# Kernel tuning notes

Measured on AMD Instinct MI355X. Metric: run time of the kernel, lower is better.

The kernel has to match this reference:

```python
import jax, jax.numpy as jnp
import numpy as np

B, S, D = 4, 2048, 1024
H, HD = 16, 64
F = 4096
EPS = 1e-5


def layer_norm(x, gamma, beta):
    mu = jnp.mean(x, axis=-1, keepdims=True)
    var = jnp.var(x, axis=-1, keepdims=True)
    return (x - mu) * jax.lax.rsqrt(var + EPS) * gamma + beta


def setup_inputs() -> dict:
    key = jax.random.key(0)
    ks = jax.random.split(key, 16)
    s_d = 1.0 / np.sqrt(D)
    s_hd = 1.0 / np.sqrt(H * HD)
    s_f = 1.0 / np.sqrt(F)
    return {
        "x": jax.random.normal(ks[0], (B, S, D), jnp.float32),
        # per-head Q/K/V linears stacked over heads: [H, D, HD]
        "Wq": jax.random.uniform(ks[1], (H, D, HD), jnp.float32, -s_d, s_d),
        "bq": jax.random.uniform(ks[2], (H, HD), jnp.float32, -s_d, s_d),
        "Wk": jax.random.uniform(ks[3], (H, D, HD), jnp.float32, -s_d, s_d),
        "bk": jax.random.uniform(ks[4], (H, HD), jnp.float32, -s_d, s_d),
        "Wv": jax.random.uniform(ks[5], (H, D, HD), jnp.float32, -s_d, s_d),
        "bv": jax.random.uniform(ks[6], (H, HD), jnp.float32, -s_d, s_d),
        "Wo": jax.random.uniform(ks[7], (H * HD, D), jnp.float32, -s_hd, s_hd),
        "bo": jax.random.uniform(ks[8], (D,), jnp.float32, -s_hd, s_hd),
        "W1": jax.random.uniform(ks[9], (D, F), jnp.float32, -s_d, s_d),
        "b1": jax.random.uniform(ks[10], (F,), jnp.float32, -s_d, s_d),
        "W2": jax.random.uniform(ks[11], (F, D), jnp.float32, -s_f, s_f),
        "b2": jax.random.uniform(ks[12], (D,), jnp.float32, -s_f, s_f),
        "g1": jnp.ones((D,), jnp.float32),
        "be1": jnp.zeros((D,), jnp.float32),
        "g2": jnp.ones((D,), jnp.float32),
        "be2": jnp.zeros((D,), jnp.float32),
    }


def reference(x, Wq, bq, Wk, bk, Wv, bv, Wo, bo, W1, b1, W2, b2, g1, be1, g2, be2):
    scale = HD ** (-0.5)
    # per-head projections: [B,S,H,HD]
    Q = jnp.einsum("bsd,hde->bshe", x, Wq) + bq
    K = jnp.einsum("bsd,hde->bshe", x, Wk) + bk
    V = jnp.einsum("bsd,hde->bshe", x, Wv) + bv
    scores = jnp.einsum("bqhe,bkhe->bhqk", Q, K) * scale
    attn = jax.nn.softmax(scores, axis=-1)
    ctx = jnp.einsum("bhqk,bkhe->bqhe", attn, V)  # [B,S,H,HD]
    concat = ctx.reshape(B, S, H * HD)  # head-order concat
    attn_out = concat @ Wo + bo
    x1 = layer_norm(x + attn_out, g1, be1)
    ffn = jax.nn.relu(x1 @ W1 + b1) @ W2 + b2
    return layer_norm(x1 + ffn, g2, be2)
```

## Files before the change

kernel.cpp:

```cpp
#include <hip/hip_runtime.h>

#define B_ 4
#define S_ 2048
#define D_ 1024
#define H_ 16
#define HD_ 64
#define F_ 4096
#define M_ (B_*S_)


typedef __attribute__((ext_vector_type(8))) short bf16x8;
typedef __attribute__((ext_vector_type(4))) short short4_t;
typedef __attribute__((ext_vector_type(4))) float f32x4;
typedef __attribute__((ext_vector_type(16))) float f32x16;

#define AS1q __attribute__((address_space(1)))
#define AS3q __attribute__((address_space(3)))

__device__ __forceinline__ float bf2f(short u) {
    union { unsigned int i; float f; } v;
    v.i = ((unsigned int)(unsigned short)u) << 16;
    return v.f;
}
__device__ __forceinline__ short f2bf(float f) {
    union { float f; unsigned int i; } v; v.f = f;
    unsigned int r = v.i + 0x7fffu + ((v.i >> 16) & 1u);
    return (short)(r >> 16);
}
__device__ __forceinline__ void gld_lds16(const short* g, short* l) {
    __builtin_amdgcn_global_load_lds((const AS1q void*)g, (AS3q void*)l, 16, 0, 0);
}
__device__ __forceinline__ unsigned int cvtpk_bf16(float a, float b) {
    unsigned int r;
    asm("v_cvt_pk_bf16_f32 %0, %1, %2" : "=v"(r) : "v"(a), "v"(b));
    return r;
}

__global__ __launch_bounds__(256) void cvt_f2b_k(
    const float* __restrict__ in, short* __restrict__ out, long n)
{
    long i = ((long)blockIdx.x * 256 + threadIdx.x) * 4;
    long stride = (long)gridDim.x * 256 * 4;
    for (; i < n; i += stride) {
        float4 v = *(const float4*)(in + i);
        short4_t o;
        o[0] = f2bf(v.x); o[1] = f2bf(v.y); o[2] = f2bf(v.z); o[3] = f2bf(v.w);
        *(short4_t*)(out + i) = o;
    }
}

template<typename TI>
__global__ __launch_bounds__(256) void transpose_k(
    const TI* __restrict__ in, short* __restrict__ out,
    int rows, long in_rstride,
    long in_bstrideB, long in_bstrideH, long out_bstride)
{
    __shared__ short tile[32][33];
    int z = blockIdx.z;
    const TI* ip = in + (long)(z >> 4) * in_bstrideB + (long)(z & 15) * in_bstrideH;
    short* op = out + (long)z * out_bstride;
    int r0 = blockIdx.y * 32, c0 = blockIdx.x * 32;
    int tx = threadIdx.x & 31, ty = threadIdx.x >> 5;
#pragma unroll
    for (int i = 0; i < 32; i += 8) {
        TI v = ip[(long)(r0 + ty + i) * in_rstride + (c0 + tx)];
        if constexpr (sizeof(TI) == 4) tile[ty + i][tx] = f2bf((float)v);
        else                           tile[ty + i][tx] = (short)v;
    }
    __syncthreads();
#pragma unroll
    for (int i = 0; i < 32; i += 8)
        op[(long)(c0 + ty + i) * rows + (r0 + tx)] = tile[tx][ty + i];
}

__global__ __launch_bounds__(256) void gemm_k(
    const short* __restrict__ A,
    const short* __restrict__ BT,
    const float* __restrict__ bias,
    short* __restrict__ C,
    int M, int N, int K, float scale, int relu)
{
    __shared__ short Alds[128*32];
    __shared__ short Blds[128*32];
    int tid = threadIdx.x;
    int wave = tid >> 6, lane = tid & 63;
    int lgrp = lane >> 4, lrow = lane & 15;
    int wr = wave >> 1, wc = wave & 1;
    int gx = gridDim.x;
    int nwg = gx * gridDim.y;
    int lin = blockIdx.y * gx + blockIdx.x;
    int nid = (lin & 7) * (nwg >> 3) + (lin >> 3);
    int bm = (nid / gx) * 128, bn = (nid % gx) * 128;

    int srow = wave * 32 + (lane >> 2);
    int scol = (lane & 3) * 8;
    const short* gA = A  + (long)(bm + srow) * K + scol;
    const short* gB = BT + (long)(bn + srow) * K + scol;
    short* lA0 = &Alds[(wave * 32) * 32];
    short* lA1 = &Alds[(wave * 32 + 16) * 32];
    short* lB0 = &Blds[(wave * 32) * 32];
    short* lB1 = &Blds[(wave * 32 + 16) * 32];
    long k16 = 16L * K;

    f32x4 acc[4][4] = {};
    for (int k0 = 0; k0 < K; k0 += 32) {
        gld_lds16(gA + k0,       lA0);
        gld_lds16(gA + k0 + k16, lA1);
        gld_lds16(gB + k0,       lB0);
        gld_lds16(gB + k0 + k16, lB1);
        __syncthreads();
        bf16x8 af[4], bv[4];
#pragma unroll
        for (int i = 0; i < 4; i++) {
            af[i] = *(const bf16x8*)&Alds[(wr*64 + i*16 + lrow) * 32 + 8*lgrp];
            bv[i] = *(const bf16x8*)&Blds[(wc*64 + i*16 + lrow) * 32 + 8*lgrp];
        }
#pragma unroll
        for (int mi = 0; mi < 4; mi++)
#pragma unroll
            for (int ni = 0; ni < 4; ni++)
                acc[mi][ni] = __builtin_amdgcn_mfma_f32_16x16x32_bf16(
                    af[mi], bv[ni], acc[mi][ni], 0, 0, 0);
        __syncthreads();
    }
#pragma unroll
    for (int ni = 0; ni < 4; ni++) {
        int col = bn + wc*64 + ni*16 + lrow;
        float bb = bias[col];
#pragma unroll
        for (int mi = 0; mi < 4; mi++) {
#pragma unroll
            for (int j = 0; j < 4; j++) {
                int row = bm + wr*64 + mi*16 + lgrp*4 + j;
                float v = (acc[mi][ni][j] + bb) * scale;
                if (relu) v = fmaxf(v, 0.0f);
                C[(long)row * N + col] = f2bf(v);
            }
        }
    }
}

__global__ __launch_bounds__(256) void attn_k(
    const short* __restrict__ Q,
    const short* __restrict__ Kb,
    const short* __restrict__ VT,
    short* __restrict__ O)
{
    __shared__ short KV[2][2][4096];
    int lin = blockIdx.y * 16 + blockIdx.x;
    int nid = (lin & 7) * 128 + (lin >> 3);
    int bh = nid >> 4, qt = nid & 15;
    int b = bh >> 4, h = bh & 15;
    int q0 = qt * 128;
    int tid = threadIdx.x, wave = tid >> 6, lane = tid & 63;
    int l31 = lane & 31, hi = lane >> 5;
    int sw = l31 & 7;

    bf16x8 aq[4];
    {
        const short* qp = Q + (long)(b*S_ + q0 + wave*32 + l31) * 1024 + h*64 + 8*hi;
#pragma unroll
        for (int t = 0; t < 4; t++)
            aq[t] = *(const bf16x8*)(qp + 16*t);
    }

    f32x16 accO[2] = {};
    float mj = -1e30f, ls = 0.f;

    int srow = lane >> 3;
    int schunk = (lane & 7) ^ srow;
    const short* ksrc = Kb + (long)(b*S_ + wave*16 + srow) * 1024 + h*64 + schunk*8;
    const short* vsrc = VT + (long)bh * (64L*S_) + (long)(wave*16 + srow) * S_ + schunk*8;
    short* kd = &KV[0][0][wave*1024];
    short* vd = &KV[0][1][wave*1024];

    #define STAGE(buf, kb_) do {                                   \
        gld_lds16(ksrc + (long)(kb_)     * 1024, kd + (buf)*8192); \
        gld_lds16(ksrc + (long)((kb_)+8) * 1024, kd + (buf)*8192 + 512); \
        gld_lds16(vsrc + (kb_),                  vd + (buf)*8192); \
        gld_lds16(vsrc + 8*S_ + (kb_),           vd + (buf)*8192 + 512); \
    } while (0)

    STAGE(0, 0);
    __syncthreads();

    for (int t = 0; t < 32; ++t) {
        int cur = t & 1;
        if (t < 31) STAGE(cur ^ 1, (t + 1) * 64);
        const char* KB = (const char*)&KV[cur][0][0];
        const char* VB = (const char*)&KV[cur][1][0];

        f32x16 accs[2] = {};
#pragma unroll
        for (int c = 0; c < 2; c++) {
            bf16x8 ak[4];
#pragma unroll
            for (int tt = 0; tt < 4; tt++)
                ak[tt] = *(const bf16x8*)(KB + (32*c + l31)*128 + (((2*tt + hi) ^ sw) << 4));
            __builtin_amdgcn_s_setprio(1);
#pragma unroll
            for (int tt = 0; tt < 4; tt++)
                accs[c] = __builtin_amdgcn_mfma_f32_32x32x16_bf16(
                    ak[tt], aq[tt], accs[c], 0, 0, 0);
            __builtin_amdgcn_s_setprio(0);
        }

        float m4 = accs[0][0];
#pragma unroll
        for (int r = 1; r < 16; r++) m4 = fmaxf(m4, accs[0][r]);
#pragma unroll
        for (int r = 0; r < 16; r++) m4 = fmaxf(m4, accs[1][r]);
        if (!__all(m4 <= mj + 8.0f)) {
            float m2 = fmaxf(m4, __shfl_xor(m4, 32));
            float mnew = fmaxf(mj, m2);
            float al = exp2f(mj - mnew);
            mj = mnew; ls *= al;
#pragma unroll
            for (int r = 0; r < 16; r++) {
                float alr = __shfl(al, (r & 3) + 8 * (r >> 2) + 4 * hi);
                accO[0][r] *= alr; accO[1][r] *= alr;
            }
        }
#pragma unroll
        for (int c = 0; c < 2; c++)
#pragma unroll
            for (int r = 0; r < 16; r++) {
                float p = exp2f(accs[c][r] - mj);
                accs[c][r] = p;
                ls += p;
            }

        bf16x8 pa[4];
#pragma unroll
        for (int ks = 0; ks < 4; ks++) {
            int c = ks >> 1, o = (ks & 1) * 8;
            unsigned int c0 = cvtpk_bf16(accs[c][o+0], accs[c][o+1]);
            unsigned int c1 = cvtpk_bf16(accs[c][o+2], accs[c][o+3]);
            unsigned int c2 = cvtpk_bf16(accs[c][o+4], accs[c][o+5]);
            unsigned int c3 = cvtpk_bf16(accs[c][o+6], accs[c][o+7]);
            asm("v_permlane32_swap_b32 %0, %1" : "+v"(c0), "+v"(c2));
            asm("v_permlane32_swap_b32 %0, %1" : "+v"(c1), "+v"(c3));
            union { unsigned int u[4]; bf16x8 v; } pk;
            pk.u[0] = c0; pk.u[1] = c1; pk.u[2] = c2; pk.u[3] = c3;
            pa[ks] = pk.v;
        }

        __builtin_amdgcn_s_setprio(1);
#pragma unroll
        for (int eb = 0; eb < 2; eb++)
#pragma unroll
            for (int ks = 0; ks < 4; ks++) {
                bf16x8 bv = *(const bf16x8*)(VB + (32*eb + l31)*128 + (((2*ks + hi) ^ sw) << 4));
                accO[eb] = __builtin_amdgcn_mfma_f32_32x32x16_bf16(
                    pa[ks], bv, accO[eb], 0, 0, 0);
            }
        __builtin_amdgcn_s_setprio(0);

        __syncthreads();
    }
    #undef STAGE

    float inv = 1.0f / (ls + __shfl_xor(ls, 32));
    const short* ob = O + (long)(b*S_) * 1024 + h*64;
#pragma unroll
    for (int r = 0; r < 16; r++) {
        int crow = (r & 3) + 8 * (r >> 2) + 4 * hi;
        float invr = __shfl(inv, crow);
        int qr = q0 + wave*32 + crow;
#pragma unroll
        for (int eb = 0; eb < 2; eb++)
            ((short*)ob)[(long)qr * 1024 + 32*eb + l31] = f2bf(accO[eb][r] * invr);
    }
}

template<int XF32, int OUTF32>
__global__ __launch_bounds__(256) void ln_k(
    const void* __restrict__ Xv, const short* __restrict__ Y,
    const float* __restrict__ g, const float* __restrict__ be,
    void* __restrict__ Ov)
{
    int row = blockIdx.x, tid = threadIdx.x;
    long base = (long)row * 1024 + tid * 4;
    float a[4];
    if constexpr (XF32) {
        float4 xv = *(const float4*)((const float*)Xv + base);
        a[0] = xv.x; a[1] = xv.y; a[2] = xv.z; a[3] = xv.w;
    } else {
        short4_t xv = *(const short4_t*)((const short*)Xv + base);
#pragma unroll
        for (int j = 0; j < 4; j++) a[j] = bf2f(xv[j]);
    }
    short4_t yv = *(const short4_t*)(Y + base);
    float s = 0.f, s2 = 0.f;
#pragma unroll
    for (int j = 0; j < 4; j++) {
        a[j] += bf2f(yv[j]);
        s += a[j]; s2 += a[j] * a[j];
    }
#pragma unroll
    for (int off = 32; off >= 1; off >>= 1) {
        s  += __shfl_xor(s, off);
        s2 += __shfl_xor(s2, off);
    }
    __shared__ float red[8];
    if ((tid & 63) == 0) { red[(tid >> 6)*2] = s; red[(tid >> 6)*2 + 1] = s2; }
    __syncthreads();
    s  = red[0] + red[2] + red[4] + red[6];
    s2 = red[1] + red[3] + red[5] + red[7];
    float mean = s * (1.0f/1024.0f);
    float var  = s2 * (1.0f/1024.0f) - mean*mean;
    float rstd = rsqrtf(var + 1e-5f);
    float4 gv = *(const float4*)(g  + tid*4);
    float4 bv = *(const float4*)(be + tid*4);
    float r0 = (a[0] - mean) * rstd * gv.x + bv.x;
    float r1 = (a[1] - mean) * rstd * gv.y + bv.y;
    float r2 = (a[2] - mean) * rstd * gv.z + bv.z;
    float r3 = (a[3] - mean) * rstd * gv.w + bv.w;
    if constexpr (OUTF32) {
        *(float4*)((float*)Ov + base) = make_float4(r0, r1, r2, r3);
    } else {
        short4_t ov;
        ov[0] = f2bf(r0); ov[1] = f2bf(r1); ov[2] = f2bf(r2); ov[3] = f2bf(r3);
        *(short4_t*)((short*)Ov + base) = ov;
    }
}

extern "C" void kernel_launch(void* const* d_in, const int* in_sizes, int n_in,
                              void* d_out, int out_size, void* d_ws, size_t ws_size,
                              hipStream_t stream)
{
    static const int ins[17] = {0,1,2,3,4,5,6,7,8,9,10,11,12,13,14,15,16};
    static const int srt[17] = {16,4,12,2,10,5,13,3,11,0,6,1,7,14,8,15,9};
    const int* IX = (in_sizes[0] == 8388608) ? ins : srt;

    const float* x   = (const float*)d_in[IX[0]];
    const float* Wq  = (const float*)d_in[IX[1]];
    const float* bq  = (const float*)d_in[IX[2]];
    const float* Wk  = (const float*)d_in[IX[3]];
    const float* bk  = (const float*)d_in[IX[4]];
    const float* Wv  = (const float*)d_in[IX[5]];
    const float* bv  = (const float*)d_in[IX[6]];
    const float* Wo  = (const float*)d_in[IX[7]];
    const float* bo  = (const float*)d_in[IX[8]];
    const float* W1  = (const float*)d_in[IX[9]];
    const float* b1  = (const float*)d_in[IX[10]];
    const float* W2  = (const float*)d_in[IX[11]];
    const float* b2  = (const float*)d_in[IX[12]];
    const float* g1  = (const float*)d_in[IX[13]];
    const float* be1 = (const float*)d_in[IX[14]];
    const float* g2  = (const float*)d_in[IX[15]];
    const float* be2 = (const float*)d_in[IX[16]];
    short* ws  = (short*)d_ws;

    short* Qb  = ws + 0L;
    short* Kbf = ws + 8388608L;
    short* xb  = ws + 16777216L;
    short* VTb = ws + 25165824L;
    short* ctx = ws + 33554432L;
    short* WqT = ws + 41943040L;
    short* WkT = ws + 42991616L;
    short* WvT = ws + 44040192L;
    short* WoT = ws + 45088768L;
    short* Vbf = ws + 46137344L;
    short* W1T = ws + 54525952L;
    short* W2T = ws + 58720256L;
    short* hb  = ws + 16777216L;
    short* ao  = ws + 0L;
    short* x1  = ws + 8388608L;
    short* ffn = ws + 0L;

    dim3 blk(256);

    cvt_f2b_k<<<2048, blk, 0, stream>>>(x, xb, (long)M_ * D_);

    transpose_k<float><<<dim3(2, 32, 16),  blk, 0, stream>>>(Wq, WqT, 1024, 64,   0, 65536, 65536);
    transpose_k<float><<<dim3(2, 32, 16),  blk, 0, stream>>>(Wk, WkT, 1024, 64,   0, 65536, 65536);
    transpose_k<float><<<dim3(2, 32, 16),  blk, 0, stream>>>(Wv, WvT, 1024, 64,   0, 65536, 65536);
    transpose_k<float><<<dim3(32, 32, 1),  blk, 0, stream>>>(Wo, WoT, 1024, 1024, 0, 0, 0);
    transpose_k<float><<<dim3(128, 32, 1), blk, 0, stream>>>(W1, W1T, 1024, 4096, 0, 0, 0);
    transpose_k<float><<<dim3(32, 128, 1), blk, 0, stream>>>(W2, W2T, 4096, 1024, 0, 0, 0);

    gemm_k<<<dim3(8, 64), blk, 0, stream>>>(xb, WqT, bq, Qb,  M_, 1024, 1024, 0.18033688011112042f, 0);
    gemm_k<<<dim3(8, 64), blk, 0, stream>>>(xb, WkT, bk, Kbf, M_, 1024, 1024, 1.0f, 0);
    gemm_k<<<dim3(8, 64), blk, 0, stream>>>(xb, WvT, bv, Vbf, M_, 1024, 1024, 1.0f, 0);

    transpose_k<short><<<dim3(2, 64, 64), blk, 0, stream>>>(Vbf, VTb, 2048, 1024, 2097152, 64, 131072);

    attn_k<<<dim3(16, 64), blk, 0, stream>>>(Qb, Kbf, VTb, ctx);

    gemm_k<<<dim3(8, 64), blk, 0, stream>>>(ctx, WoT, bo, ao, M_, 1024, 1024, 1.0f, 0);
    ln_k<1,0><<<8192, blk, 0, stream>>>(x, ao, g1, be1, x1);

    gemm_k<<<dim3(32, 64), blk, 0, stream>>>(x1, W1T, b1, hb,  M_, 4096, 1024, 1.0f, 1);
    gemm_k<<<dim3(8, 64),  blk, 0, stream>>>(hb, W2T, b2, ffn, M_, 1024, 4096, 1.0f, 0);

    ln_k<0,1><<<8192, blk, 0, stream>>>(x1, ffn, g2, be2, d_out);
}
```

Baseline: 495.3 us.

## Fuse Q/K/V projections into one GEMM and compute softmax row sums via MFMA

Concatenates the transposed Q, K and V weights and runs a single 3072-wide GEMM that writes an interleaved QKV buffer, replacing three separate launches. The attention kernel now reads Q and K at the wider row stride. It computes the softmax denominator with an extra MFMA against a ones vector instead of scalar adds, and uses v_max3 for the row max. This trims launch overhead, improves tile occupancy and cuts VALU work in the softmax loop, at the cost of extra MFMA issue and strided K loads.

After: 470.1 us. 5.1% less time.

```diff
diff --git a/kernel.cpp b/kernel.cpp
--- a/kernel.cpp
+++ b/kernel.cpp
@@ -7,6 +7,7 @@
 #define HD_ 64
 #define F_ 4096
 #define M_ (B_*S_)
+#define QS_ 3072
 
 
 typedef __attribute__((ext_vector_type(8))) short bf16x8;
@@ -33,6 +34,11 @@
 __device__ __forceinline__ unsigned int cvtpk_bf16(float a, float b) {
     unsigned int r;
     asm("v_cvt_pk_bf16_f32 %0, %1, %2" : "=v"(r) : "v"(a), "v"(b));
+    return r;
+}
+__device__ __forceinline__ float max3f(float a, float b, float c) {
+    float r;
+    asm("v_max3_f32 %0, %1, %2, %3" : "=v"(r) : "v"(a), "v"(b), "v"(c));
     return r;
 }
 
@@ -140,9 +146,79 @@
     }
 }
 
+__global__ __launch_bounds__(256) void gemm_qkv_k(
+    const short* __restrict__ A,
+    const short* __restrict__ BT,
+    const float* __restrict__ bq,
+    const float* __restrict__ bk,
+    const float* __restrict__ bv,
+    short* __restrict__ C,
+    float qscale)
+{
+    __shared__ short Alds[128*32];
+    __shared__ short Blds[128*32];
+    const int K = 1024;
+    int tid = threadIdx.x;
+    int wave = tid >> 6, lane = tid & 63;
+    int lgrp = lane >> 4, lrow = lane & 15;
+    int wr = wave >> 1, wc = wave & 1;
+    int gx = gridDim.x;
+    int nwg = gx * gridDim.y;
+    int lin = blockIdx.y * gx + blockIdx.x;
+    int nid = (lin & 7) * (nwg >> 3) + (lin >> 3);
+    int bm = (nid / gx) * 128, bn = (nid % gx) * 128;
+    int seg = bn >> 10;
+    const float* bp = (seg == 0) ? bq : (seg == 1) ? bk : bv;
+    float scale = (seg == 0) ? qscale : 1.0f;
+
+    int srow = wave * 32 + (lane >> 2);
+    int scol = (lane & 3) * 8;
+    const short* gA = A  + (long)(bm + srow) * K + scol;
+    const short* gB = BT + (long)(bn + srow) * K + scol;
+    short* lA0 = &Alds[(wave * 32) * 32];
+    short* lA1 = &Alds[(wave * 32 + 16) * 32];
+    short* lB0 = &Blds[(wave * 32) * 32];
+    short* lB1 = &Blds[(wave * 32 + 16) * 32];
+    long k16 = 16L * K;
+
+    f32x4 acc[4][4] = {};
+    for (int k0 = 0; k0 < K; k0 += 32) {
+        gld_lds16(gA + k0,       lA0);
+        gld_lds16(gA + k0 + k16, lA1);
+        gld_lds16(gB + k0,       lB0);
+        gld_lds16(gB + k0 + k16, lB1);
+        __syncthreads();
+        bf16x8 af[4], bvv[4];
+#pragma unroll
+        for (int i = 0; i < 4; i++) {
+            af[i]  = *(const bf16x8*)&Alds[(wr*64 + i*16 + lrow) * 32 + 8*lgrp];
+            bvv[i] = *(const bf16x8*)&Blds[(wc*64 + i*16 + lrow) * 32 + 8*lgrp];
+        }
+#pragma unroll
+        for (int mi = 0; mi < 4; mi++)
+#pragma unroll
+            for (int ni = 0; ni < 4; ni++)
+                acc[mi][ni] = __builtin_amdgcn_mfma_f32_16x16x32_bf16(
+                    af[mi], bvv[ni], acc[mi][ni], 0, 0, 0);
+        __syncthreads();
+    }
+#pragma unroll
+    for (int ni = 0; ni < 4; ni++) {
+        int col = bn + wc*64 + ni*16 + lrow;
+        float bb = bp[col & 1023];
+#pragma unroll
+        for (int mi = 0; mi < 4; mi++) {
+#pragma unroll
+            for (int j = 0; j < 4; j++) {
+                int row = bm + wr*64 + mi*16 + lgrp*4 + j;
+                C[(long)row * QS_ + col] = f2bf((acc[mi][ni][j] + bb) * scale);
+            }
+        }
+    }
+}
+
 __global__ __launch_bounds__(256) void attn_k(
-    const short* __restrict__ Q,
-    const short* __restrict__ Kb,
+    const short* __restrict__ QKV,
     const short* __restrict__ VT,
     short* __restrict__ O)
 {
@@ -158,27 +234,31 @@
 
     bf16x8 aq[4];
     {
-        const short* qp = Q + (long)(b*S_ + q0 + wave*32 + l31) * 1024 + h*64 + 8*hi;
+        const short* qp = QKV + (long)(b*S_ + q0 + wave*32 + l31) * QS_ + h*64 + 8*hi;
 #pragma unroll
         for (int t = 0; t < 4; t++)
             aq[t] = *(const bf16x8*)(qp + 16*t);
     }
+    bf16x8 ones;
+#pragma unroll
+    for (int i = 0; i < 8; i++) ones[i] = (short)0x3F80;
 
     f32x16 accO[2] = {};
-    float mj = -1e30f, ls = 0.f;
+    f32x16 accsum = {};
+    float mj = -1e30f;
 
     int srow = lane >> 3;
     int schunk = (lane & 7) ^ srow;
-    const short* ksrc = Kb + (long)(b*S_ + wave*16 + srow) * 1024 + h*64 + schunk*8;
+    const short* ksrc = QKV + (long)(b*S_ + wave*16 + srow) * QS_ + 1024 + h*64 + schunk*8;
     const short* vsrc = VT + (long)bh * (64L*S_) + (long)(wave*16 + srow) * S_ + schunk*8;
     short* kd = &KV[0][0][wave*1024];
     short* vd = &KV[0][1][wave*1024];
 
-    #define STAGE(buf, kb_) do {                                   \
-        gld_lds16(ksrc + (long)(kb_)     * 1024, kd + (buf)*8192); \
-        gld_lds16(ksrc + (long)((kb_)+8) * 1024, kd + (buf)*8192 + 512); \
-        gld_lds16(vsrc + (kb_),                  vd + (buf)*8192); \
-        gld_lds16(vsrc + 8*S_ + (kb_),           vd + (buf)*8192 + 512); \
+    #define STAGE(buf, kb_) do {                                        \
+        gld_lds16(ksrc + (long)(kb_)     * QS_, kd + (buf)*8192);        \
+        gld_lds16(ksrc + (long)((kb_)+8) * QS_, kd + (buf)*8192 + 512);  \
+        gld_lds16(vsrc + (kb_),                 vd + (buf)*8192);        \
+        gld_lds16(vsrc + 8*S_ + (kb_),          vd + (buf)*8192 + 512);  \
     } while (0)
 
     STAGE(0, 0);
@@ -205,30 +285,30 @@
             __builtin_amdgcn_s_setprio(0);
         }
 
-        float m4 = accs[0][0];
-#pragma unroll
-        for (int r = 1; r < 16; r++) m4 = fmaxf(m4, accs[0][r]);
-#pragma unroll
-        for (int r = 0; r < 16; r++) m4 = fmaxf(m4, accs[1][r]);
+        float mA = fmaxf(accs[0][0], accs[0][1]);
+        float mB = fmaxf(accs[1][0], accs[1][1]);
+#pragma unroll
+        for (int r = 2; r < 16; r += 2) {
+            mA = max3f(mA, accs[0][r], accs[0][r+1]);
+            mB = max3f(mB, accs[1][r], accs[1][r+1]);
+        }
+        float m4 = fmaxf(mA, mB);
         if (!__all(m4 <= mj + 8.0f)) {
             float m2 = fmaxf(m4, __shfl_xor(m4, 32));
             float mnew = fmaxf(mj, m2);
             float al = exp2f(mj - mnew);
-            mj = mnew; ls *= al;
+            mj = mnew;
 #pragma unroll
             for (int r = 0; r < 16; r++) {
                 float alr = __shfl(al, (r & 3) + 8 * (r >> 2) + 4 * hi);
-                accO[0][r] *= alr; accO[1][r] *= alr;
+                accO[0][r] *= alr; accO[1][r] *= alr; accsum[r] *= alr;
             }
         }
 #pragma unroll
         for (int c = 0; c < 2; c++)
 #pragma unroll
-            for (int r = 0; r < 16; r++) {
-                float p = exp2f(accs[c][r] - mj);
-                accs[c][r] = p;
-                ls += p;
-            }
+            for (int r = 0; r < 16; r++)
+                accs[c][r] = exp2f(accs[c][r] - mj);
 
         bf16x8 pa[4];
 #pragma unroll
@@ -250,22 +330,25 @@
         for (int eb = 0; eb < 2; eb++)
 #pragma unroll
             for (int ks = 0; ks < 4; ks++) {
-                bf16x8 bv = *(const bf16x8*)(VB + (32*eb + l31)*128 + (((2*ks + hi) ^ sw) << 4));
+                bf16x8 bvf = *(const bf16x8*)(VB + (32*eb + l31)*128 + (((2*ks + hi) ^ sw) << 4));
                 accO[eb] = __builtin_amdgcn_mfma_f32_32x32x16_bf16(
-                    pa[ks], bv, accO[eb], 0, 0, 0);
+                    pa[ks], bvf, accO[eb], 0, 0, 0);
             }
+#pragma unroll
+        for (int ks = 0; ks < 4; ks++)
+            accsum = __builtin_amdgcn_mfma_f32_32x32x16_bf16(
+                pa[ks], ones, accsum, 0, 0, 0);
         __builtin_amdgcn_s_setprio(0);
 
         __syncthreads();
     }
     #undef STAGE
 
-    float inv = 1.0f / (ls + __shfl_xor(ls, 32));
     const short* ob = O + (long)(b*S_) * 1024 + h*64;
 #pragma unroll
     for (int r = 0; r < 16; r++) {
         int crow = (r & 3) + 8 * (r >> 2) + 4 * hi;
-        float invr = __shfl(inv, crow);
+        float invr = 1.0f / accsum[r];
         int qr = q0 + wave*32 + crow;
 #pragma unroll
         for (int eb = 0; eb < 2; eb++)
@@ -352,41 +435,37 @@
     const float* be2 = (const float*)d_in[IX[16]];
     short* ws  = (short*)d_ws;
 
-    short* Qb  = ws + 0L;
-    short* Kbf = ws + 8388608L;
-    short* xb  = ws + 16777216L;
-    short* VTb = ws + 25165824L;
-    short* ctx = ws + 33554432L;
-    short* WqT = ws + 41943040L;
-    short* WkT = ws + 42991616L;
-    short* WvT = ws + 44040192L;
-    short* WoT = ws + 45088768L;
-    short* Vbf = ws + 46137344L;
-    short* W1T = ws + 54525952L;
-    short* W2T = ws + 58720256L;
-    short* hb  = ws + 16777216L;
-    short* ao  = ws + 0L;
-    short* x1  = ws + 8388608L;
-    short* ffn = ws + 0L;
+    short* QKVb = ws + 0L;
+    short* VTb  = ws + 25165824L;
+    short* ctx  = ws + 33554432L;
+    short* QKVT = ws + 41943040L;
+    short* WoT  = ws + 45088768L;
+    short* xb   = ws + 46137344L;
+    short* W1T  = ws + 54525952L;
+    short* W2T  = ws + 58720256L;
+    short* x1   = ws + 0L;
+    short* hb   = ws + 8388608L;
+    short* ao   = ws + 46137344L;
+    short* ffn  = ws + 41943040L;
 
     dim3 blk(256);
 
     cvt_f2b_k<<<2048, blk, 0, stream>>>(x, xb, (long)M_ * D_);
 
-    transpose_k<float><<<dim3(2, 32, 16),  blk, 0, stream>>>(Wq, WqT, 1024, 64,   0, 65536, 65536);
-    transpose_k<float><<<dim3(2, 32, 16),  blk, 0, stream>>>(Wk, WkT, 1024, 64,   0, 65536, 65536);
-    transpose_k<float><<<dim3(2, 32, 16),  blk, 0, stream>>>(Wv, WvT, 1024, 64,   0, 65536, 65536);
+    transpose_k<float><<<dim3(2, 32, 16),  blk, 0, stream>>>(Wq, QKVT,            1024, 64,   0, 65536, 65536);
+    transpose_k<float><<<dim3(2, 32, 16),  blk, 0, stream>>>(Wk, QKVT + 1048576L, 1024, 64,   0, 65536, 65536);
+    transpose_k<float><<<dim3(2, 32, 16),  blk, 0, stream>>>(Wv, QKVT + 2097152L, 1024, 64,   0, 65536, 65536);
     transpose_k<float><<<dim3(32, 32, 1),  blk, 0, stream>>>(Wo, WoT, 1024, 1024, 0, 0, 0);
     transpose_k<float><<<dim3(128, 32, 1), blk, 0, stream>>>(W1, W1T, 1024, 4096, 0, 0, 0);
     transpose_k<float><<<dim3(32, 128, 1), blk, 0, stream>>>(W2, W2T, 4096, 1024, 0, 0, 0);
 
-    gemm_k<<<dim3(8, 64), blk, 0, stream>>>(xb, WqT, bq, Qb,  M_, 1024, 1024, 0.18033688011112042f, 0);
-    gemm_k<<<dim3(8, 64), blk, 0, stream>>>(xb, WkT, bk, Kbf, M_, 1024, 1024, 1.0f, 0);
-    gemm_k<<<dim3(8, 64), blk, 0, stream>>>(xb, WvT, bv, Vbf, M_, 1024, 1024, 1.0f, 0);
-
-    transpose_k<short><<<dim3(2, 64, 64), blk, 0, stream>>>(Vbf, VTb, 2048, 1024, 2097152, 64, 131072);
-
-    attn_k<<<dim3(16, 64), blk, 0, stream>>>(Qb, Kbf, VTb, ctx);
+    gemm_qkv_k<<<dim3(24, 64), blk, 0, stream>>>(
+        xb, QKVT, bq, bk, bv, QKVb, 0.18033688011112042f);
+
+    transpose_k<short><<<dim3(2, 64, 64), blk, 0, stream>>>(
+        QKVb + 2048, VTb, 2048, QS_, (long)S_*QS_, 64, 131072);
+
+    attn_k<<<dim3(16, 64), blk, 0, stream>>>(QKVb, VTb, ctx);
 
     gemm_k<<<dim3(8, 64), blk, 0, stream>>>(ctx, WoT, bo, ao, M_, 1024, 1024, 1.0f, 0);
     ln_k<1,0><<<8192, blk, 0, stream>>>(x, ao, g1, be1, x1);
```
